# Optimization experiments

Measured on AMD Instinct MI355X. Metric: run time of the kernel, lower is better.

Reference implementation:

```python
import jax, jax.numpy as jnp
import numpy as np

WIDTH = 1.0  # radial_width
AMPLITUDE = (WIDTH ** 0.5) * 1.772637204826652  # ~sqrt(pi*width)
BN_EPS = 1e-3  # keras BatchNormalization default


def sine_pos_encoding(seq_len, hidden, dtype):
    # keras_nlp.layers.SinePositionEncoding, max_wavelength=10000
    position = jnp.arange(seq_len, dtype=dtype)
    min_freq = jnp.asarray(1.0 / 10000.0, dtype)
    timescales = min_freq ** (2 * (jnp.arange(hidden) // 2).astype(dtype) / hidden)
    angles = position[:, None] * timescales[None, :]  # [T, H]
    odd = (jnp.arange(hidden) % 2).astype(dtype)
    return jnp.sin(angles) * (1 - odd) + jnp.cos(angles) * odd


def setup_inputs() -> dict:
    key = jax.random.key(0)
    ks = jax.random.split(key, 4)
    B, T, C, F, K, L = 16, 4096, 8, 64, 11, 4096
    x = jax.random.normal(ks[0], (B, T, C), jnp.float32)
    conv_w = jax.random.normal(ks[1], (K, C, F), jnp.float32) * 0.1
    conv_b = jnp.zeros((F,), jnp.float32)
    gamma = jnp.ones((F,), jnp.float32)
    beta = jnp.zeros((F,), jnp.float32)
    mean = jnp.zeros((F,), jnp.float32)
    var = jnp.ones((F,), jnp.float32)
    # HeNormal init for dense
    dense_w = jax.random.normal(ks[2], (F, L), jnp.float32) * (2.0 / F) ** 0.5
    dense_b = jnp.zeros((L,), jnp.float32)
    return dict(x=x, conv_w=conv_w, conv_b=conv_b, gamma=gamma, beta=beta,
                mean=mean, var=var, dense_w=dense_w, dense_b=dense_b)


def reference(x, conv_w, conv_b, gamma, beta, mean, var, dense_w, dense_b):
    B, T, C = x.shape
    F = conv_w.shape[-1]
    L = dense_w.shape[-1]
    # Conv1D same padding -> [B, T, F]
    h = jax.lax.conv_general_dilated(x, conv_w, (1,), 'SAME',
                                     dimension_numbers=('NWC', 'WIO', 'NWC')) + conv_b
    # BatchNorm (inference form)
    h = (h - mean) / jnp.sqrt(var + BN_EPS) * gamma + beta
    # Softmax over time axis
    h = jax.nn.softmax(h, axis=1)
    # sine positional encoding added
    h = h + sine_pos_encoding(T, F, x.dtype)
    # Dense with sigmoid, rescale to [-1, 1]
    d = jax.nn.sigmoid(h @ dense_w + dense_b) * 2.0 - 1.0  # [B, T, L]
    # ReductionLayer: sum over time -> shift weights [B, L]
    shift = jnp.sum(d, axis=1)
    # ShiftingLayer: Gaussian RBF warp matrix then matmul
    idx_in = jnp.arange(1, T + 1, dtype=x.dtype)                       # [T]
    scale = jnp.asarray(T / L, x.dtype)
    idx_sh = (jnp.arange(1, L + 1, dtype=x.dtype) + shift) * scale     # [B, L]
    M = idx_in[None, None, :] - idx_sh[:, :, None]                     # [B, L, T]
    M = jnp.exp(-(M * M) / WIDTH) / AMPLITUDE
    return jnp.matmul(M, x)  # [B, L, C]
```

## Files before the change

### kernel.cpp

```cpp
#include <hip/hip_runtime.h>
#include <stdint.h>

#define BB 16
#define TT 4096
#define CC 8
#define FF 64
#define KW 11
#define LL 4096

#define L2E 1.442695040888963f

typedef __attribute__((ext_vector_type(8))) short short8;
typedef __attribute__((ext_vector_type(16))) float floatx16;

__device__ __forceinline__ unsigned short f2b(float f) {
    union { float f; uint32_t i; } v; v.f = f;
    uint32_t x = v.i;
    return (unsigned short)((x + 0x7fffu + ((x >> 16) & 1u)) >> 16);
}
__device__ __forceinline__ float b2f(unsigned short u) {
    union { uint32_t i; float f; } v; v.i = ((uint32_t)u) << 16; return v.f;
}

__global__ __launch_bounds__(256) void k_split(
        const float* __restrict__ dw, unsigned short* __restrict__ Wt) {
    const int idx  = blockIdx.x * 256 + threadIdx.x;
    const int j    = idx & 7;
    const int ln   = (idx >> 3) & 31;
    const int half = (idx >> 8) & 1;
    const int kf   = (idx >> 9) & 3;
    const int lt   = idx >> 11;
    const int l = lt * 32 + ln;
    const int k = kf * 16 + half * 8 + j;
    const float v = dw[(size_t)k * LL + l];
    const unsigned short hi = f2b(v);
    const unsigned short lo = f2b(v - b2f(hi));
    Wt[idx] = hi;
    Wt[262144 + idx] = lo;
}

__global__ __launch_bounds__(256) void k_sumexp(
        const float* __restrict__ x, const float* __restrict__ cw,
        const float* __restrict__ cb, const float* __restrict__ gm,
        const float* __restrict__ bt, const float* __restrict__ mn,
        const float* __restrict__ vr, float* __restrict__ sumexp) {
    __shared__ __align__(16) float xsm[(64 + KW - 1) * CC];
    __shared__ float red[4 * FF];
    const int tid = threadIdx.x;
    const int b  = blockIdx.x / (TT / 64);
    const int t0 = (blockIdx.x % (TT / 64)) * 64;
    const int f = tid & 63, ts = tid >> 6;

    float wreg[KW * CC];
#pragma unroll
    for (int kc = 0; kc < KW * CC; ++kc) wreg[kc] = cw[kc * FF + f];

    for (int i = tid; i < (64 + KW - 1) * CC; i += 256) {
        int row = i >> 3, c = i & 7;
        int t = t0 - (KW / 2) + row;
        xsm[i] = (t >= 0 && t < TT) ? x[((size_t)b * TT + t) * CC + c] : 0.0f;
    }
    const float s  = gm[f] * rsqrtf(vr[f] + 1e-3f);
    const float bb = bt[f] + (cb[f] - mn[f]) * s;
    const float s2 = s * L2E, b2 = bb * L2E;
    __syncthreads();

    const float4* xv = (const float4*)xsm;
    float esum = 0.f;
#pragma unroll 2
    for (int i = 0; i < 16; ++i) {
        const int tt = ts + 4 * i;
        float acc = 0.f;
#pragma unroll
        for (int k = 0; k < KW; ++k) {
            const float4 xa = xv[(tt + k) * 2];
            const float4 xb = xv[(tt + k) * 2 + 1];
            acc = fmaf(xa.x, wreg[k * 8 + 0], acc);
            acc = fmaf(xa.y, wreg[k * 8 + 1], acc);
            acc = fmaf(xa.z, wreg[k * 8 + 2], acc);
            acc = fmaf(xa.w, wreg[k * 8 + 3], acc);
            acc = fmaf(xb.x, wreg[k * 8 + 4], acc);
            acc = fmaf(xb.y, wreg[k * 8 + 5], acc);
            acc = fmaf(xb.z, wreg[k * 8 + 6], acc);
            acc = fmaf(xb.w, wreg[k * 8 + 7], acc);
        }
        esum += __builtin_amdgcn_exp2f(fmaf(acc, s2, b2));
    }
    red[ts * FF + f] = esum;
    __syncthreads();
    if (ts == 0) {
        float tot = red[f] + red[FF + f] + red[2 * FF + f] + red[3 * FF + f];
        atomicAdd(&sumexp[b * FF + f], tot);
    }
}

__global__ __launch_bounds__(512) void k_main(
        const float* __restrict__ x,  const float* __restrict__ cw,
        const float* __restrict__ cb, const float* __restrict__ gm,
        const float* __restrict__ bt, const float* __restrict__ mn,
        const float* __restrict__ vr, const unsigned short* __restrict__ Wt,
        const float* __restrict__ db, const float* __restrict__ sumexp,
        float* __restrict__ shiftsum) {
    __shared__ __align__(16) unsigned short As[16384];
    __shared__ __align__(16) float xsm[(128 + KW - 1) * CC];

    const int tid = threadIdx.x;
    const int b  = blockIdx.y;
    const int t0 = blockIdx.x * 128;
    const int f = tid & 63, tq = tid >> 6;

    float wreg[KW * CC];
#pragma unroll
    for (int kc = 0; kc < KW * CC; ++kc) wreg[kc] = cw[kc * FF + f];

    for (int i = tid; i < (128 + KW - 1) * CC; i += 512) {
        int row = i >> 3, c = i & 7;
        int t = t0 - (KW / 2) + row;
        xsm[i] = (t >= 0 && t < TT) ? x[((size_t)b * TT + t) * CC + c] : 0.0f;
    }
    const float s   = gm[f] * rsqrtf(vr[f] + 1e-3f);
    const float bbv = bt[f] + (cb[f] - mn[f]) * s;
    const float s2 = s * L2E, b2 = bbv * L2E;
    const float inv_se = 1.0f / sumexp[b * FF + f];
    const float tsf = exp2f(-0.20762050586796017f * (float)(f & ~1));
    const int kfh = ((f >> 4) << 1) | ((f >> 3) & 1);
    const int jj  = f & 7;
    const float ang0 = (float)(t0 + tq) * tsf;
    const float dA = 8.0f * tsf;
    float sv = sinf(ang0), cv = cosf(ang0);
    const float sd = sinf(dA), cd = cosf(dA);
    __syncthreads();

    const float4* xv = (const float4*)xsm;
#pragma unroll 2
    for (int i = 0; i < 16; ++i) {
        const int tt = tq + 8 * i;
        float acc = 0.f;
#pragma unroll
        for (int k = 0; k < KW; ++k) {
            const float4 xa = xv[(tt + k) * 2];
            const float4 xb = xv[(tt + k) * 2 + 1];
            acc = fmaf(xa.x, wreg[k * 8 + 0], acc);
            acc = fmaf(xa.y, wreg[k * 8 + 1], acc);
            acc = fmaf(xa.z, wreg[k * 8 + 2], acc);
            acc = fmaf(xa.w, wreg[k * 8 + 3], acc);
            acc = fmaf(xb.x, wreg[k * 8 + 4], acc);
            acc = fmaf(xb.y, wreg[k * 8 + 5], acc);
            acc = fmaf(xb.z, wreg[k * 8 + 6], acc);
            acc = fmaf(xb.w, wreg[k * 8 + 7], acc);
        }
        float e = __builtin_amdgcn_exp2f(fmaf(acc, s2, b2));
        float p = (f & 1) ? cv : sv;
        float h = fmaf(e, inv_se, p);
        const unsigned short hi = f2b(h);
        const unsigned short lo = f2b(h - b2f(hi));
        const int off = ((tt >> 5) * 8 + kfh) * 256 + (tt & 31) * 8 + jj;
        As[off] = hi;
        As[8192 + off] = lo;
        float ns = fmaf(sv, cd, cv * sd);
        float nc = fmaf(cv, cd, -(sv * sd));
        sv = ns; cv = nc;
    }
    __syncthreads();

    const int lane = tid & 63;
    const int wv   = tid >> 6;
    const int half = lane >> 5;
    const int ln31 = lane & 31;
    const int vbase = (half << 9) | (ln31 << 4);
    const char* Ab = (const char*)As;
    const char* Wb = (const char*)Wt;

#pragma unroll 1
    for (int lt = 0; lt < 16; ++lt) {
        const int ltile = lt * 8 + wv;
        const int lbase = ltile * 32;
        const char* wp = Wb + ((size_t)ltile << 12) + vbase;
        short8 Whi[4], Wlo[4];
#pragma unroll
        for (int kf = 0; kf < 4; ++kf) {
            Whi[kf] = *reinterpret_cast<const short8*>(wp + kf * 1024);
            Wlo[kf] = *reinterpret_cast<const short8*>(wp + 524288 + kf * 1024);
        }
        const float dbn = db[lbase + ln31] * (-L2E);

        float ss[4] = {0.f, 0.f, 0.f, 0.f};
#pragma unroll
        for (int nt = 0; nt < 4; ++nt) {
            floatx16 acc = {0.f, 0.f, 0.f, 0.f, 0.f, 0.f, 0.f, 0.f,
                            0.f, 0.f, 0.f, 0.f, 0.f, 0.f, 0.f, 0.f};
#pragma unroll
            for (int kf = 0; kf < 4; ++kf) {
                const int ao = (nt * 8 + kf * 2) << 9;
                short8 Ahi = *reinterpret_cast<const short8*>(Ab + ao + vbase);
                short8 Alo = *reinterpret_cast<const short8*>(Ab + 16384 + ao + vbase);
                acc = __builtin_amdgcn_mfma_f32_32x32x16_bf16(Ahi, Whi[kf], acc, 0, 0, 0);
                acc = __builtin_amdgcn_mfma_f32_32x32x16_bf16(Alo, Whi[kf], acc, 0, 0, 0);
                acc = __builtin_amdgcn_mfma_f32_32x32x16_bf16(Ahi, Wlo[kf], acc, 0, 0, 0);
            }
#pragma unroll
            for (int q = 0; q < 4; ++q) {
                float e0 = __builtin_amdgcn_exp2f(fmaf(acc[4 * q + 0], -L2E, dbn));
                float e1 = __builtin_amdgcn_exp2f(fmaf(acc[4 * q + 1], -L2E, dbn));
                float e2 = __builtin_amdgcn_exp2f(fmaf(acc[4 * q + 2], -L2E, dbn));
                float e3 = __builtin_amdgcn_exp2f(fmaf(acc[4 * q + 3], -L2E, dbn));
                float a0 = 1.f + e0, a1 = 1.f + e1, a2 = 1.f + e2, a3 = 1.f + e3;
                float p01 = a0 * a1, p23 = a2 * a3;
                float num = fmaf(a0 + a1, p23, (a2 + a3) * p01);
                ss[q] = fmaf(num, __builtin_amdgcn_rcpf(p01 * p23), ss[q]);
            }
        }
        float ssum = (ss[0] + ss[1]) + (ss[2] + ss[3]);
        ssum += __shfl_xor(ssum, 32);
        if (half == 0)
            atomicAdd(shiftsum + (size_t)b * LL + lbase + ln31, ssum);
    }
}

__global__ __launch_bounds__(256) void k_warp(
        const float* __restrict__ shiftsum, const float* __restrict__ x,
        float* __restrict__ out) {
    const int idx = blockIdx.x * 256 + threadIdx.x;
    const int l = idx & (LL - 1);
    const int b = idx >> 12;
    const float sh = fmaf(2.0f, shiftsum[idx], -(float)TT);
    const float scale = (float)TT / (float)LL;
    const float center = ((float)(l + 1) + sh) * scale;
    const float R = 7.0f;
    int tlo = (int)ceilf(center - 1.0f - R);
    int thi = (int)floorf(center - 1.0f + R);
    if (tlo < 0) tlo = 0;
    if (thi > TT - 1) thi = TT - 1;
    float acc[CC];
#pragma unroll
    for (int c = 0; c < CC; ++c) acc[c] = 0.f;
    const float inv_amp = (float)(1.0 / 1.772637204826652);
    for (int t = tlo; t <= thi; ++t) {
        float d = (float)(t + 1) - center;
        float w = __expf(-d * d) * inv_amp;
        const float4 x0 = *reinterpret_cast<const float4*>(x + ((size_t)b * TT + t) * CC);
        const float4 x1 = *reinterpret_cast<const float4*>(x + ((size_t)b * TT + t) * CC + 4);
        acc[0] = fmaf(w, x0.x, acc[0]);
        acc[1] = fmaf(w, x0.y, acc[1]);
        acc[2] = fmaf(w, x0.z, acc[2]);
        acc[3] = fmaf(w, x0.w, acc[3]);
        acc[4] = fmaf(w, x1.x, acc[4]);
        acc[5] = fmaf(w, x1.y, acc[5]);
        acc[6] = fmaf(w, x1.z, acc[6]);
        acc[7] = fmaf(w, x1.w, acc[7]);
    }
    float* o = out + (size_t)idx * CC;
    *reinterpret_cast<float4*>(o)     = make_float4(acc[0], acc[1], acc[2], acc[3]);
    *reinterpret_cast<float4*>(o + 4) = make_float4(acc[4], acc[5], acc[6], acc[7]);
}

extern "C" void kernel_launch(void* const* d_in, const int* in_sizes, int n_in,
                              void* d_out, int out_size, void* d_ws, size_t ws_size,
                              hipStream_t stream) {
    const float* x  = (const float*)d_in[0];
    const float* cw = (const float*)d_in[1];
    const float* cb = (const float*)d_in[2];
    const float* gm = (const float*)d_in[3];
    const float* bt = (const float*)d_in[4];
    const float* mn = (const float*)d_in[5];
    const float* vr = (const float*)d_in[6];
    const float* dw = (const float*)d_in[7];
    const float* db = (const float*)d_in[8];

    float* sumexp      = (float*)d_ws;
    float* shiftsum    = sumexp + BB * FF;
    unsigned short* Wt = (unsigned short*)(shiftsum + BB * LL);

    hipMemsetAsync(sumexp, 0, (size_t)(BB * FF + BB * LL) * sizeof(float), stream);

    k_split<<<(FF * LL) / 256, 256, 0, stream>>>(dw, Wt);
    k_sumexp<<<BB * (TT / 64), 256, 0, stream>>>(x, cw, cb, gm, bt, mn, vr, sumexp);
    k_main<<<dim3(TT / 128, BB), 512, 0, stream>>>(x, cw, cb, gm, bt, mn, vr,
                                                   Wt, db, sumexp, shiftsum);
    k_warp<<<(BB * LL) / 256, 256, 0, stream>>>(shiftsum, x, (float*)d_out);
}
```

Baseline: 217.8 us.

## Store conv exp results in global buffer instead of recomputing in main kernel

The first pass now writes exp(BN(conv)) for every (b,t,f) to a 16 MB global buffer. The main kernel reads these values back instead of recomputing the 11-tap convolution. The main kernel also staggers each wave's L-tile start order and raises wave priority around the MFMA block. This trades redundant conv FLOPs for extra global memory write and read traffic.

```diff
diff --git a/kernel.cpp b/kernel.cpp
--- a/kernel.cpp
+++ b/kernel.cpp
@@ -12,6 +12,8 @@
 
 typedef __attribute__((ext_vector_type(8))) short short8;
 typedef __attribute__((ext_vector_type(16))) float floatx16;
+
+__device__ float e_buf[(size_t)BB * TT * FF];
 
 __device__ __forceinline__ unsigned short f2b(float f) {
     union { float f; uint32_t i; } v; v.f = f;
@@ -39,7 +41,7 @@
     Wt[262144 + idx] = lo;
 }
 
-__global__ __launch_bounds__(256) void k_sumexp(
+__global__ __launch_bounds__(256) void k_conv(
         const float* __restrict__ x, const float* __restrict__ cw,
         const float* __restrict__ cb, const float* __restrict__ gm,
         const float* __restrict__ bt, const float* __restrict__ mn,
@@ -65,76 +67,12 @@
     const float s2 = s * L2E, b2 = bb * L2E;
     __syncthreads();
 
+    float* eb = e_buf + ((size_t)b * TT + t0) * FF + f;
     const float4* xv = (const float4*)xsm;
     float esum = 0.f;
 #pragma unroll 2
     for (int i = 0; i < 16; ++i) {
         const int tt = ts + 4 * i;
-        float acc = 0.f;
-#pragma unroll
-        for (int k = 0; k < KW; ++k) {
-            const float4 xa = xv[(tt + k) * 2];
-            const float4 xb = xv[(tt + k) * 2 + 1];
-            acc = fmaf(xa.x, wreg[k * 8 + 0], acc);
-            acc = fmaf(xa.y, wreg[k * 8 + 1], acc);
-            acc = fmaf(xa.z, wreg[k * 8 + 2], acc);
-            acc = fmaf(xa.w, wreg[k * 8 + 3], acc);
-            acc = fmaf(xb.x, wreg[k * 8 + 4], acc);
-            acc = fmaf(xb.y, wreg[k * 8 + 5], acc);
-            acc = fmaf(xb.z, wreg[k * 8 + 6], acc);
-            acc = fmaf(xb.w, wreg[k * 8 + 7], acc);
-        }
-        esum += __builtin_amdgcn_exp2f(fmaf(acc, s2, b2));
-    }
-    red[ts * FF + f] = esum;
-    __syncthreads();
-    if (ts == 0) {
-        float tot = red[f] + red[FF + f] + red[2 * FF + f] + red[3 * FF + f];
-        atomicAdd(&sumexp[b * FF + f], tot);
-    }
-}
-
-__global__ __launch_bounds__(512) void k_main(
-        const float* __restrict__ x,  const float* __restrict__ cw,
-        const float* __restrict__ cb, const float* __restrict__ gm,
-        const float* __restrict__ bt, const float* __restrict__ mn,
-        const float* __restrict__ vr, const unsigned short* __restrict__ Wt,
-        const float* __restrict__ db, const float* __restrict__ sumexp,
-        float* __restrict__ shiftsum) {
-    __shared__ __align__(16) unsigned short As[16384];
-    __shared__ __align__(16) float xsm[(128 + KW - 1) * CC];
-
-    const int tid = threadIdx.x;
-    const int b  = blockIdx.y;
-    const int t0 = blockIdx.x * 128;
-    const int f = tid & 63, tq = tid >> 6;
-
-    float wreg[KW * CC];
-#pragma unroll
-    for (int kc = 0; kc < KW * CC; ++kc) wreg[kc] = cw[kc * FF + f];
-
-    for (int i = tid; i < (128 + KW - 1) * CC; i += 512) {
-        int row = i >> 3, c = i & 7;
-        int t = t0 - (KW / 2) + row;
-        xsm[i] = (t >= 0 && t < TT) ? x[((size_t)b * TT + t) * CC + c] : 0.0f;
-    }
-    const float s   = gm[f] * rsqrtf(vr[f] + 1e-3f);
-    const float bbv = bt[f] + (cb[f] - mn[f]) * s;
-    const float s2 = s * L2E, b2 = bbv * L2E;
-    const float inv_se = 1.0f / sumexp[b * FF + f];
-    const float tsf = exp2f(-0.20762050586796017f * (float)(f & ~1));
-    const int kfh = ((f >> 4) << 1) | ((f >> 3) & 1);
-    const int jj  = f & 7;
-    const float ang0 = (float)(t0 + tq) * tsf;
-    const float dA = 8.0f * tsf;
-    float sv = sinf(ang0), cv = cosf(ang0);
-    const float sd = sinf(dA), cd = cosf(dA);
-    __syncthreads();
-
-    const float4* xv = (const float4*)xsm;
-#pragma unroll 2
-    for (int i = 0; i < 16; ++i) {
-        const int tt = tq + 8 * i;
         float acc = 0.f;
 #pragma unroll
         for (int k = 0; k < KW; ++k) {
@@ -150,8 +88,46 @@
             acc = fmaf(xb.w, wreg[k * 8 + 7], acc);
         }
         float e = __builtin_amdgcn_exp2f(fmaf(acc, s2, b2));
+        eb[tt * FF] = e;
+        esum += e;
+    }
+    red[ts * FF + f] = esum;
+    __syncthreads();
+    if (ts == 0) {
+        float tot = red[f] + red[FF + f] + red[2 * FF + f] + red[3 * FF + f];
+        atomicAdd(&sumexp[b * FF + f], tot);
+    }
+}
+
+__global__ __launch_bounds__(512) void k_main(
+        const float* __restrict__ gm,  const float* __restrict__ bt,
+        const float* __restrict__ mn,  const float* __restrict__ vr,
+        const unsigned short* __restrict__ Wt,
+        const float* __restrict__ db,  const float* __restrict__ sumexp,
+        float* __restrict__ shiftsum) {
+    __shared__ __align__(16) unsigned short As[16384];
+
+    const int tid = threadIdx.x;
+    const int b  = blockIdx.y;
+    const int t0 = blockIdx.x * 128;
+    const int f = tid & 63, tq = tid >> 6;
+
+    const float inv_se = 1.0f / sumexp[b * FF + f];
+    const float tsf = exp2f(-0.20762050586796017f * (float)(f & ~1));
+    const int kfh = ((f >> 4) << 1) | ((f >> 3) & 1);
+    const int jj  = f & 7;
+    const float ang0 = (float)(t0 + tq) * tsf;
+    const float dA = 8.0f * tsf;
+    float sv = sinf(ang0), cv = cosf(ang0);
+    const float sd = sinf(dA), cd = cosf(dA);
+
+    const float* eb = e_buf + ((size_t)b * TT + t0) * FF + f;
+#pragma unroll 4
+    for (int i = 0; i < 16; ++i) {
+        const int tt = tq + 8 * i;
+        float ev = eb[tt * FF];
         float p = (f & 1) ? cv : sv;
-        float h = fmaf(e, inv_se, p);
+        float h = fmaf(ev, inv_se, p);
         const unsigned short hi = f2b(h);
         const unsigned short lo = f2b(h - b2f(hi));
         const int off = ((tt >> 5) * 8 + kfh) * 256 + (tt & 31) * 8 + jj;
@@ -172,7 +148,8 @@
     const char* Wb = (const char*)Wt;
 
 #pragma unroll 1
-    for (int lt = 0; lt < 16; ++lt) {
+    for (int i = 0; i < 16; ++i) {
+        const int lt = (i + 2 * wv) & 15;
         const int ltile = lt * 8 + wv;
         const int lbase = ltile * 32;
         const char* wp = Wb + ((size_t)ltile << 12) + vbase;
@@ -189,6 +166,7 @@
         for (int nt = 0; nt < 4; ++nt) {
             floatx16 acc = {0.f, 0.f, 0.f, 0.f, 0.f, 0.f, 0.f, 0.f,
                             0.f, 0.f, 0.f, 0.f, 0.f, 0.f, 0.f, 0.f};
+            __builtin_amdgcn_s_setprio(1);
 #pragma unroll
             for (int kf = 0; kf < 4; ++kf) {
                 const int ao = (nt * 8 + kf * 2) << 9;
@@ -198,6 +176,7 @@
                 acc = __builtin_amdgcn_mfma_f32_32x32x16_bf16(Alo, Whi[kf], acc, 0, 0, 0);
                 acc = __builtin_amdgcn_mfma_f32_32x32x16_bf16(Ahi, Wlo[kf], acc, 0, 0, 0);
             }
+            __builtin_amdgcn_s_setprio(0);
 #pragma unroll
             for (int q = 0; q < 4; ++q) {
                 float e0 = __builtin_amdgcn_exp2f(fmaf(acc[4 * q + 0], -L2E, dbn));
@@ -274,8 +253,8 @@
     hipMemsetAsync(sumexp, 0, (size_t)(BB * FF + BB * LL) * sizeof(float), stream);
 
     k_split<<<(FF * LL) / 256, 256, 0, stream>>>(dw, Wt);
-    k_sumexp<<<BB * (TT / 64), 256, 0, stream>>>(x, cw, cb, gm, bt, mn, vr, sumexp);
-    k_main<<<dim3(TT / 128, BB), 512, 0, stream>>>(x, cw, cb, gm, bt, mn, vr,
+    k_conv<<<BB * (TT / 64), 256, 0, stream>>>(x, cw, cb, gm, bt, mn, vr, sumexp);
+    k_main<<<dim3(TT / 128, BB), 512, 0, stream>>>(gm, bt, mn, vr,
                                                    Wt, db, sumexp, shiftsum);
     k_warp<<<(BB * LL) / 256, 256, 0, stream>>>(shiftsum, x, (float*)d_out);
 }
```

Result: faster. 206.3 us (-5.3%).
